# Performance work log

Measured on AMD Instinct MI355X. Metric: run time of the kernel, lower is better.

## Reference

```python
import jax, jax.numpy as jnp
import numpy as np

N, DIM = 100000, 512
HID = DIM // 2


def _mlp(z, W1, b1, W2, b2):
    # shared scorer: [N, dim] -> [N, 1]
    h = jax.nn.relu(z @ W1 + b1)
    return h @ W2 + b2


def setup_inputs() -> dict:
    key = jax.random.key(0)
    k1, k2, k3, k4 = jax.random.split(key, 4)
    s1 = 1.0 / np.sqrt(DIM)
    s2 = 1.0 / np.sqrt(HID)
    return {
        "z1": jax.random.normal(k1, (N, DIM), dtype=jnp.float32),
        "z2": jax.random.normal(k2, (N, DIM), dtype=jnp.float32),
        "W1": jax.random.normal(k3, (DIM, HID), dtype=jnp.float32) * s1,
        "b1": jnp.zeros((HID,), dtype=jnp.float32),
        "W2": jax.random.normal(k4, (HID, 1), dtype=jnp.float32) * s2,
        "b2": jnp.zeros((1,), dtype=jnp.float32),
    }


def reference(z1, z2, W1, b1, W2, b2):
    x = _mlp(z1, W1, b1, W2, b2)  # [N, 1]
    y = _mlp(z2, W1, b1, W2, b2)  # [N, 1]
    # exp-normalize pair: score_x = e^x / (e^x + e^y) == sigmoid(x - y)
    # computed exactly as in the original (plain exp, no max-subtract)
    e_x = jnp.exp(x)
    e_y = jnp.exp(y)
    denom = e_x + e_y
    score_x = e_x / denom  # [N, 1]
    score_y = e_y / denom  # [N, 1]
    # diag(score) @ z  ==  score * z  (row-wise broadcast scale)
    return score_x * z1 + score_y * z2
```

## Files before the change

kernel.cpp:

```cpp
#include <hip/hip_runtime.h>
#include <hip/hip_bf16.h>
#include <cmath>

#define DIM 512
#define HID 256
#define ROWS_PB 16
#define NCHUNK 16
#define CB 16384

typedef __attribute__((ext_vector_type(8))) short short8;
typedef __attribute__((ext_vector_type(4))) float f32x4;
typedef __attribute__((ext_vector_type(4))) unsigned int u32x4;

__device__ __forceinline__ unsigned short f2bf(float f) {
  union { float f; unsigned u; } v; v.f = f;
  unsigned u = v.u;
  return (unsigned short)((u + 0x7FFFu + ((u >> 16) & 1u)) >> 16);
}
__device__ __forceinline__ float bf2f(short h) {
  union { unsigned u; float f; } v;
  v.u = ((unsigned)(unsigned short)h) << 16;
  return v.f;
}

__global__ void w1_swz_kernel(const float* __restrict__ W1,
                              unsigned short* __restrict__ w1s) {
  int tid = blockIdx.x * blockDim.x + threadIdx.x;
  if (tid >= DIM * HID) return;
  int k = tid / HID;
  int c = tid - k * HID;
  w1s[(((k >> 3) * HID) + c) * 8 + (k & 7)] = f2bf(W1[tid]);
}

__device__ __forceinline__ short8 cvt8(const f32x4 p0, const f32x4 p1) {
  short8 r;
  r[0] = (short)f2bf(p0[0]); r[1] = (short)f2bf(p0[1]);
  r[2] = (short)f2bf(p0[2]); r[3] = (short)f2bf(p0[3]);
  r[4] = (short)f2bf(p1[0]); r[5] = (short)f2bf(p1[1]);
  r[6] = (short)f2bf(p1[2]); r[7] = (short)f2bf(p1[3]);
  return r;
}

__device__ __forceinline__ void wcombine(float wa, const short8 a, float wb,
                                         const short8 b, f32x4& o0, f32x4& o1) {
#pragma unroll
  for (int i = 0; i < 4; ++i) {
    o0[i] = wa * bf2f(a[i]) + wb * bf2f(b[i]);
    o1[i] = wa * bf2f(a[i + 4]) + wb * bf2f(b[i + 4]);
  }
}

__global__ __launch_bounds__(256, 2) void fa_main_kernel(
    const float* __restrict__ z1, const float* __restrict__ z2,
    const unsigned short* __restrict__ w1s,
    const float* __restrict__ bias1, const float* __restrict__ W2,
    const float* __restrict__ bias2, float* __restrict__ out, int n) {
  __shared__ short8 Az[2 * NCHUNK * 64];
  __shared__ char Bbuf[2][CB];
  __shared__ float xs2[2][2][ROWS_PB];

  const int t = threadIdx.x;
  const int w = t >> 6;
  const int l = t & 63;
  const int l15 = l & 15, l16 = l >> 4;
  const int s = w & 1;
  const int h = w >> 1;
  const int row0 = blockIdx.x * ROWS_PB;
  const int myrow = row0 + l15;
  const bool rok = myrow < n;
  const float* zz = s ? z2 : z1;
  const float* ap = zz + (size_t)myrow * DIM + (l16 << 3);
  const f32x4 zf4 = (f32x4){0.f, 0.f, 0.f, 0.f};

  u32x4 breg0, breg1, breg2, breg3;
#define BLOAD(c)                                            \
  {                                                         \
    const u32x4* g = (const u32x4*)w1s + (c) * 1024 + t;    \
    breg0 = g[0];                                           \
    breg1 = g[256];                                         \
    breg2 = g[512];                                         \
    breg3 = g[768];                                         \
  }
#define BWRITE(c)                                           \
  {                                                         \
    u32x4* d = (u32x4*)&Bbuf[(c) & 1][0] + t;               \
    d[0] = breg0;                                           \
    d[256] = breg1;                                         \
    d[512] = breg2;                                         \
    d[768] = breg3;                                         \
  }

  BLOAD(0);
  __builtin_amdgcn_sched_barrier(0);
  {
    f32x4 pp[8][2];
#pragma unroll
    for (int j = 0; j < 8; ++j) {
      const float* p = ap + ((h * 8 + j) << 5);
      pp[j][0] = rok ? *(const f32x4*)(p) : zf4;
      pp[j][1] = rok ? *(const f32x4*)(p + 4) : zf4;
    }
    BWRITE(0);
#pragma unroll
    for (int j = 0; j < 8; ++j)
      Az[(s * NCHUNK + h * 8 + j) * 64 + l] = cvt8(pp[j][0], pp[j][1]);
  }
  __syncthreads();

  short8 af[NCHUNK];
#pragma unroll
  for (int c = 0; c < NCHUNK; ++c) af[c] = Az[(s * NCHUNK + c) * 64 + l];

  f32x4 acc[8];
#pragma unroll
  for (int f = 0; f < 8; ++f) acc[f] = zf4;

#pragma unroll
  for (int c = 0; c < NCHUNK; ++c) {
    if (c + 1 < NCHUNK) BLOAD(c + 1);
    __builtin_amdgcn_sched_barrier(0);
    const short8* bp =
        (const short8*)&Bbuf[c & 1][0] + (l16 << 8) + (h << 7) + l15;
#pragma unroll
    for (int f = 0; f < 8; ++f) {
      const short8 bf = bp[f << 4];
      acc[f] =
          __builtin_amdgcn_mfma_f32_16x16x32_bf16(af[c], bf, acc[f], 0, 0, 0);
    }
    if (c + 1 < NCHUNK) BWRITE(c + 1);
    __syncthreads();
  }

  float part[4] = {0.f, 0.f, 0.f, 0.f};
#pragma unroll
  for (int f = 0; f < 8; ++f) {
    const int cc = (h << 7) + (f << 4) + l15;
    const float w2v = W2[cc];
    const float b1v = bias1[cc];
#pragma unroll
    for (int r = 0; r < 4; ++r) {
      const float hh = acc[f][r] + b1v;
      part[r] += (hh > 0.f) ? hh * w2v : 0.f;
    }
  }
#pragma unroll
  for (int r = 0; r < 4; ++r) {
#pragma unroll
    for (int m = 1; m < 16; m <<= 1) part[r] += __shfl_xor(part[r], m, 16);
  }
  if (l15 == 0) {
#pragma unroll
    for (int r = 0; r < 4; ++r) xs2[s][h][(l16 << 2) + r] = part[r];
  }
  __syncthreads();

  const float x = xs2[0][0][l15] + xs2[0][1][l15];
  const float y = xs2[1][0][l15] + xs2[1][1][l15];
  const float d = y - x;
  const float sx = 1.f / (1.f + __expf(d));
  const float sy = 1.f - sx;
  float* orow = out + (size_t)myrow * DIM + (l16 << 3);
  if (rok) {
#pragma unroll
    for (int j = 0; j < 4; ++j) {
      const int c = (w << 2) + j;
      const short8 a0 = Az[(0 * NCHUNK + c) * 64 + l];
      const short8 a1 = Az[(1 * NCHUNK + c) * 64 + l];
      f32x4 o0, o1;
      wcombine(sx, a0, sy, a1, o0, o1);
      *(f32x4*)(orow + (c << 5)) = o0;
      *(f32x4*)(orow + (c << 5) + 4) = o1;
    }
  }
#undef BLOAD
#undef BWRITE
}

extern "C" void kernel_launch(void* const* d_in, const int* in_sizes, int n_in,
                              void* d_out, int out_size, void* d_ws,
                              size_t ws_size, hipStream_t stream) {
  const float* z1 = (const float*)d_in[0];
  const float* z2 = (const float*)d_in[1];
  const float* W1 = (const float*)d_in[2];
  const float* b1 = (const float*)d_in[3];
  const float* W2 = (const float*)d_in[4];
  const float* b2 = (const float*)d_in[5];
  float* out = (float*)d_out;
  const int n = in_sizes[0] / DIM;
  unsigned short* w1s = (unsigned short*)d_ws;

  hipLaunchKernelGGL(w1_swz_kernel, dim3((DIM * HID + 255) / 256), dim3(256),
                     0, stream, W1, w1s);
  const int nwg = (n + ROWS_PB - 1) / ROWS_PB;
  hipLaunchKernelGGL(fa_main_kernel, dim3(nwg), dim3(256), 0, stream, z1, z2,
                     w1s, b1, W2, b2, out, n);
}
```

Measured before the change: 206.7 us.

## Process 32 rows per block with each wave covering all hidden columns

Doubles rows per workgroup to 32. Each wave now owns one 16-row tile for one input and computes all 256 hidden columns, instead of splitting the hidden dimension across waves. This halves how often each W1 chunk is staged per row and doubles the MFMA work per B-fragment load. The B buffer drops from double-buffered to single-buffered with an extra barrier per chunk, and the reduction scratch aliases the B region. LDS use grows to 80KB and the accumulators double to 16, which may limit occupancy and lose the load/compute overlap that double buffering gave.

Measured after the change: 187.2 us. 1.1x faster.

```diff
diff --git a/kernel.cpp b/kernel.cpp
--- a/kernel.cpp
+++ b/kernel.cpp
@@ -4,7 +4,7 @@
 
 #define DIM 512
 #define HID 256
-#define ROWS_PB 16
+#define ROWS_PB 32
 #define NCHUNK 16
 #define CB 16384
 
@@ -55,18 +55,19 @@
     const unsigned short* __restrict__ w1s,
     const float* __restrict__ bias1, const float* __restrict__ W2,
     const float* __restrict__ bias2, float* __restrict__ out, int n) {
-  __shared__ short8 Az[2 * NCHUNK * 64];
-  __shared__ char Bbuf[2][CB];
-  __shared__ float xs2[2][2][ROWS_PB];
+  __shared__ char smem[81920];
+  short8* Az = (short8*)smem;
+  char* Bs = smem + 65536;
+  float* xs = (float*)(smem + 65536);
 
   const int t = threadIdx.x;
   const int w = t >> 6;
   const int l = t & 63;
   const int l15 = l & 15, l16 = l >> 4;
   const int s = w & 1;
-  const int h = w >> 1;
+  const int tl = w >> 1;
   const int row0 = blockIdx.x * ROWS_PB;
-  const int myrow = row0 + l15;
+  const int myrow = row0 + tl * 16 + l15;
   const bool rok = myrow < n;
   const float* zz = s ? z2 : z1;
   const float* ap = zz + (size_t)myrow * DIM + (l16 << 3);
@@ -81,9 +82,9 @@
     breg2 = g[512];                                         \
     breg3 = g[768];                                         \
   }
-#define BWRITE(c)                                           \
+#define BWRITE()                                            \
   {                                                         \
-    u32x4* d = (u32x4*)&Bbuf[(c) & 1][0] + t;               \
+    u32x4* d = (u32x4*)Bs + t;                              \
     d[0] = breg0;                                           \
     d[256] = breg1;                                         \
     d[512] = breg2;                                         \
@@ -92,49 +93,50 @@
 
   BLOAD(0);
   __builtin_amdgcn_sched_barrier(0);
-  {
-    f32x4 pp[8][2];
 #pragma unroll
-    for (int j = 0; j < 8; ++j) {
-      const float* p = ap + ((h * 8 + j) << 5);
-      pp[j][0] = rok ? *(const f32x4*)(p) : zf4;
-      pp[j][1] = rok ? *(const f32x4*)(p + 4) : zf4;
+  for (int g = 0; g < 4; ++g) {
+    f32x4 p[4][2];
+#pragma unroll
+    for (int j = 0; j < 4; ++j) {
+      const float* pp = ap + (((g << 2) + j) << 5);
+      p[j][0] = rok ? *(const f32x4*)(pp) : zf4;
+      p[j][1] = rok ? *(const f32x4*)(pp + 4) : zf4;
     }
-    BWRITE(0);
 #pragma unroll
-    for (int j = 0; j < 8; ++j)
-      Az[(s * NCHUNK + h * 8 + j) * 64 + l] = cvt8(pp[j][0], pp[j][1]);
+    for (int j = 0; j < 4; ++j)
+      Az[((s * NCHUNK + (g << 2) + j) * 2 + tl) * 64 + l] =
+          cvt8(p[j][0], p[j][1]);
   }
+  BWRITE();
   __syncthreads();
 
-  short8 af[NCHUNK];
+  f32x4 acc[16];
 #pragma unroll
-  for (int c = 0; c < NCHUNK; ++c) af[c] = Az[(s * NCHUNK + c) * 64 + l];
-
-  f32x4 acc[8];
-#pragma unroll
-  for (int f = 0; f < 8; ++f) acc[f] = zf4;
+  for (int f = 0; f < 16; ++f) acc[f] = zf4;
 
 #pragma unroll
   for (int c = 0; c < NCHUNK; ++c) {
     if (c + 1 < NCHUNK) BLOAD(c + 1);
     __builtin_amdgcn_sched_barrier(0);
-    const short8* bp =
-        (const short8*)&Bbuf[c & 1][0] + (l16 << 8) + (h << 7) + l15;
+    const short8* bp = (const short8*)Bs + (l16 << 8) + l15;
+    const short8 af = Az[((s * NCHUNK + c) * 2 + tl) * 64 + l];
+    short8 bf[16];
 #pragma unroll
-    for (int f = 0; f < 8; ++f) {
-      const short8 bf = bp[f << 4];
+    for (int f = 0; f < 16; ++f) bf[f] = bp[f << 4];
+    __builtin_amdgcn_sched_barrier(0);
+#pragma unroll
+    for (int f = 0; f < 16; ++f)
       acc[f] =
-          __builtin_amdgcn_mfma_f32_16x16x32_bf16(af[c], bf, acc[f], 0, 0, 0);
-    }
-    if (c + 1 < NCHUNK) BWRITE(c + 1);
+          __builtin_amdgcn_mfma_f32_16x16x32_bf16(af, bf[f], acc[f], 0, 0, 0);
+    __syncthreads();
+    if (c + 1 < NCHUNK) BWRITE();
     __syncthreads();
   }
 
   float part[4] = {0.f, 0.f, 0.f, 0.f};
 #pragma unroll
-  for (int f = 0; f < 8; ++f) {
-    const int cc = (h << 7) + (f << 4) + l15;
+  for (int f = 0; f < 16; ++f) {
+    const int cc = (f << 4) + l15;
     const float w2v = W2[cc];
     const float b1v = bias1[cc];
 #pragma unroll
@@ -150,26 +152,26 @@
   }
   if (l15 == 0) {
 #pragma unroll
-    for (int r = 0; r < 4; ++r) xs2[s][h][(l16 << 2) + r] = part[r];
+    for (int r = 0; r < 4; ++r)
+      xs[s * ROWS_PB + tl * 16 + (l16 << 2) + r] = part[r];
   }
   __syncthreads();
 
-  const float x = xs2[0][0][l15] + xs2[0][1][l15];
-  const float y = xs2[1][0][l15] + xs2[1][1][l15];
-  const float d = y - x;
-  const float sx = 1.f / (1.f + __expf(d));
+  const float x = xs[tl * 16 + l15];
+  const float y = xs[ROWS_PB + tl * 16 + l15];
+  const float sx = 1.f / (1.f + __expf(y - x));
   const float sy = 1.f - sx;
   float* orow = out + (size_t)myrow * DIM + (l16 << 3);
   if (rok) {
 #pragma unroll
-    for (int j = 0; j < 4; ++j) {
-      const int c = (w << 2) + j;
-      const short8 a0 = Az[(0 * NCHUNK + c) * 64 + l];
-      const short8 a1 = Az[(1 * NCHUNK + c) * 64 + l];
+    for (int j = 0; j < 8; ++j) {
+      const int cc = (s << 3) + j;
+      const short8 a0 = Az[((0 * NCHUNK + cc) * 2 + tl) * 64 + l];
+      const short8 a1 = Az[((1 * NCHUNK + cc) * 2 + tl) * 64 + l];
       f32x4 o0, o1;
       wcombine(sx, a0, sy, a1, o0, o1);
-      *(f32x4*)(orow + (c << 5)) = o0;
-      *(f32x4*)(orow + (c << 5) + 4) = o1;
+      *(f32x4*)(orow + (cc << 5)) = o0;
+      *(f32x4*)(orow + (cc << 5) + 4) = o1;
     }
   }
 #undef BLOAD
```
